# Kernel optimization log

Measured on AMD Instinct MI355X. Metric: run time of the kernel, lower is better.

Reference implementation:

```python
import jax, jax.numpy as jnp
import numpy as np

N = 20000          # num proposals (nodes)
E = 320000         # num edges
IN = 4096          # roi feature dim
EMB = 200          # glove embed dim
HID = 512          # hidden dim
NH = 8             # heads (conv1)
HC = HID // NH     # 64 per-head channels
NCLS = 151         # VG object classes
NEG_SLOPE = 0.2    # PyG GATConv leaky_relu slope


def setup_inputs() -> dict:
    key = jax.random.key(0)
    ks = jax.random.split(key, 18)
    d_in1 = IN + EMB + 128  # 4424, conv1 input dim
    inp = {
        "roi_features": jax.random.normal(ks[0], (N, IN), jnp.float32),
        "box_info": jax.random.uniform(ks[1], (N, 9), jnp.float32),
        # embedding tables
        "emb1": jax.random.normal(ks[2], (NCLS, EMB), jnp.float32) * 0.02,
        "emb2": jax.random.normal(ks[3], (NCLS, EMB), jnp.float32) * 0.02,
        # bbox MLP 9 -> 32 -> 128
        "bw1": jax.random.normal(ks[4], (9, 32), jnp.float32) / np.sqrt(9),
        "bb1": jnp.zeros((32,), jnp.float32),
        "bw2": jax.random.normal(ks[5], (32, 128), jnp.float32) / np.sqrt(32),
        "bb2": jnp.zeros((128,), jnp.float32),
        # GATConv1: d_in1 -> 8 heads x 64, concat
        "W1": jax.random.normal(ks[6], (d_in1, NH * HC), jnp.float32) / np.sqrt(d_in1),
        "a_src1": jax.random.normal(ks[7], (NH, HC), jnp.float32) * 0.1,
        "a_dst1": jax.random.normal(ks[8], (NH, HC), jnp.float32) * 0.1,
        "bias1": jnp.zeros((NH * HC,), jnp.float32),
        # GATConv2: 512 -> 512, 1 head, concat=False
        "W2": jax.random.normal(ks[9], (HID, HID), jnp.float32) / np.sqrt(HID),
        "a_src2": jax.random.normal(ks[10], (1, HID), jnp.float32) * 0.1,
        "a_dst2": jax.random.normal(ks[11], (1, HID), jnp.float32) * 0.1,
        "bias2": jnp.zeros((HID,), jnp.float32),
        # int inputs
        "obj_labels": jax.random.randint(ks[12], (N,), 0, NCLS, jnp.int32),
        "edge_index": jax.random.randint(ks[13], (2, E), 0, N, jnp.int32),
    }
    return inp


def _segment_softmax(logits, seg, n):
    # logits: [E, H]; softmax over edges sharing the same destination seg id
    m = jax.ops.segment_max(logits, seg, num_segments=n)
    e = jnp.exp(logits - m[seg])
    s = jax.ops.segment_sum(e, seg, num_segments=n)
    return e / (s[seg] + 1e-16)


def _gat_conv(x, src, dst, W, a_src, a_dst, bias, concat):
    # PyG GATConv (self-loops already included in src/dst); dropout off (eval)
    n = x.shape[0]
    H, C = a_src.shape
    h = (x @ W).reshape(n, H, C)                      # [N, H, C]
    al_s = jnp.einsum('nhc,hc->nh', h, a_src)         # [N, H]
    al_d = jnp.einsum('nhc,hc->nh', h, a_dst)
    logits = jax.nn.leaky_relu(al_s[src] + al_d[dst], NEG_SLOPE)  # [E, H]
    alpha = _segment_softmax(logits, dst, n)          # [E, H]
    out = jax.ops.segment_sum(alpha[:, :, None] * h[src], dst, num_segments=n)
    out = out.reshape(n, H * C) if concat else out.mean(axis=1)
    return out + bias


def reference(roi_features, box_info, emb1, emb2, bw1, bb1, bw2, bb2,
              W1, a_src1, a_dst1, bias1, W2, a_src2, a_dst2, bias2,
              obj_labels, edge_index):
    n = roi_features.shape[0]
    # predcls mode: GT labels -> embedding lookup
    obj_embed = emb1[obj_labels]                              # [N, 200]
    pos = jax.nn.relu(box_info @ bw1 + bb1)
    pos = jax.nn.relu(pos @ bw2 + bb2)                        # [N, 128]
    x = jnp.concatenate([roi_features, obj_embed, pos], -1)  # [N, 4424]

    # add self-loops (PyG GATConv default)
    ar = jnp.arange(n, dtype=edge_index.dtype)
    src = jnp.concatenate([edge_index[0], ar])
    dst = jnp.concatenate([edge_index[1], ar])

    edge_f1 = jax.nn.elu(_gat_conv(x, src, dst, W1, a_src1, a_dst1, bias1, True))
    obj_feats = _gat_conv(edge_f1, src, dst, W2, a_src2, a_dst2, bias2, False)

    obj_dists = jax.nn.one_hot(obj_labels, NCLS, dtype=jnp.float32)
    edge_pre_rep = jnp.concatenate([roi_features, obj_feats, emb2[obj_labels]], -1)
    return obj_dists, obj_labels, edge_pre_rep
```

## Files before the change

### kernel.cpp

```cpp
#include <hip/hip_runtime.h>
#include <hip/hip_bf16.h>

#define NNODES 20000
#define NEDGES 320000
#define ETOT   (NEDGES + NNODES)
#define KPADX  4224
#define SK     4
#define KC     (KPADX / SK)
#define MPAD   20096
#define NCLS   151
#define EPRW   4808
#define OUT_LAB_OFF  3020000L
#define OUT_EPR_OFF  3040000L
#define NSLOPE 0.2f
#define NGEMM1 2512
#define NCOPY  10000

typedef __attribute__((ext_vector_type(8))) short bf16x8;
typedef __attribute__((ext_vector_type(4))) float f32x4;
typedef __attribute__((ext_vector_type(4))) short s16x4;

__device__ __forceinline__ short f2bf(float v) {
  union { __hip_bfloat16 b; short s; } u;
  u.b = __float2bfloat16(v);
  return u.s;
}

__device__ __forceinline__ float bf2f(short s) {
  union { float f; unsigned u; } x;
  x.u = ((unsigned)(unsigned short)s) << 16;
  return x.f;
}

__device__ __forceinline__ void gld16(const short* g, short* l) {
  __builtin_amdgcn_global_load_lds(
      (const __attribute__((address_space(1))) unsigned int*)g,
      (__attribute__((address_space(3))) unsigned int*)l, 16, 0, 0);
}

#define QB0 5000
#define QB1 (QB0 + 5000)
#define QB2 (QB1 + 1584)
#define QB3 (QB2 + 2112)
#define QB4 (QB3 + 256)
#define QB5 (QB4 + 1329)
#define QB6 (QB5 + 151)

__global__ __launch_bounds__(256) void mega_prep_kernel(
    const float* __restrict__ roi, const float* __restrict__ box,
    const float* __restrict__ emb1, const float* __restrict__ emb2,
    const float* __restrict__ bw1, const float* __restrict__ bb1,
    const float* __restrict__ bw2, const float* __restrict__ bb2,
    const float* __restrict__ W1, const float* __restrict__ W2,
    const int* __restrict__ labels, const int* __restrict__ ei,
    short* __restrict__ x, short* __restrict__ w1t, short* __restrict__ w2t,
    short* __restrict__ ef1, int* __restrict__ deg,
    float* __restrict__ als2, float* __restrict__ ald2,
    float* __restrict__ E1, float* __restrict__ dout) {
  const int b = blockIdx.x;
  const int tid = threadIdx.x;

  __shared__ float hids[4][32];
  __shared__ float tile[32][33];

  if (b < QB0) {
    const int c0 = b * 2048 + tid;
    f32x4 v0[8], v1[8];
#pragma unroll
    for (int k = 0; k < 8; ++k) {
      const int c = c0 + k * 256;
      const float* src = &roi[((long)(c >> 9) << 12) + (c & 511) * 8];
      v0[k] = *(const f32x4*)src;
      v1[k] = *(const f32x4*)(src + 4);
    }
#pragma unroll
    for (int k = 0; k < 8; ++k) {
      const int c = c0 + k * 256;
      bf16x8 bb;
      bb[0] = f2bf(v0[k].x); bb[1] = f2bf(v0[k].y);
      bb[2] = f2bf(v0[k].z); bb[3] = f2bf(v0[k].w);
      bb[4] = f2bf(v1[k].x); bb[5] = f2bf(v1[k].y);
      bb[6] = f2bf(v1[k].z); bb[7] = f2bf(v1[k].w);
      __builtin_nontemporal_store(bb,
          (bf16x8*)&x[(long)(c >> 9) * KPADX + (c & 511) * 8]);
    }
  } else if (b < QB1) {
    const int w = tid >> 6;
    const int lane = tid & 63;
    const int nd = (b - QB0) * 4 + w;
    if (lane < 32) {
      float a = bb1[lane];
#pragma unroll
      for (int i = 0; i < 9; ++i) a += box[nd * 9 + i] * bw1[i * 32 + lane];
      hids[w][lane] = a > 0.f ? a : 0.f;
    }
    __syncthreads();
    const long xrow = (long)nd * KPADX;
#pragma unroll
    for (int jj = 0; jj < 2; ++jj) {
      const int j = lane + jj * 64;
      float a = bb2[j];
#pragma unroll
      for (int i = 0; i < 32; ++i) a += hids[w][i] * bw2[i * 128 + j];
      a = a > 0.f ? a : 0.f;
      x[xrow + 4096 + j] = f2bf(a);
    }
    const int lab = labels[nd];
    float* epr = dout + OUT_EPR_OFF + (long)nd * EPRW;
    if (lane < 50) {
      const f32x4 e2 = *(const f32x4*)&emb2[lab * 200 + lane * 4];
      __builtin_nontemporal_store(e2, (f32x4*)&epr[4608 + lane * 4]);
    }
    for (int j = lane; j < NCLS; j += 64)
      dout[(long)nd * NCLS + j] = (j == lab) ? 1.f : 0.f;
    if (lane == 0) dout[OUT_LAB_OFF + nd] = (float)lab;
  } else if (b < QB2) {
    const int t = (b - QB1) * 256 + tid;
    if (t < 96 * KPADX) x[(long)NNODES * KPADX + t] = 0;
    if (t < 96 * 512)   ef1[(long)NNODES * 512 + t] = 0;
    if (t < MPAD)       { als2[t] = 0.f; ald2[t] = 0.f; }
  } else if (b < QB3) {
    const int t = b - QB2;
    const int n0 = (t % 16) * 32;
    const int k0 = (t / 16) * 32;
    const int tx = tid & 31, ty = tid >> 5;
#pragma unroll
    for (int i = ty; i < 32; i += 8) {
      const int kp = k0 + i;
      const int src = kp < 4096 ? kp : kp + 200;
      tile[i][tx] = W1[(long)src * 512 + (n0 + tx)];
    }
    __syncthreads();
#pragma unroll
    for (int i = ty; i < 32; i += 8)
      w1t[(long)(n0 + i) * KPADX + (k0 + tx)] = f2bf(tile[tx][i]);
  } else if (b < QB4) {
    const int t = b - QB3;
    const int n0 = (t % 16) * 32;
    const int k0 = (t / 16) * 32;
    const int tx = tid & 31, ty = tid >> 5;
#pragma unroll
    for (int i = ty; i < 32; i += 8)
      tile[i][tx] = W2[(long)(k0 + i) * 512 + (n0 + tx)];
    __syncthreads();
#pragma unroll
    for (int i = ty; i < 32; i += 8)
      w2t[(long)(n0 + i) * 512 + (k0 + tx)] = f2bf(tile[tx][i]);
  } else if (b < QB5) {
    const int e = (b - QB4) * 256 + tid;
    if (e < ETOT) {
      const int d = (e < NEDGES) ? ei[NEDGES + e] : (e - NEDGES);
      atomicAdd(&deg[d], 1);
    }
  } else {
    const int c = b - QB5;
#pragma unroll
    for (int jj = 0; jj < 2; ++jj) {
      const int j = tid + jj * 256;
      float a = 0.f;
      for (int k = 0; k < 200; ++k)
        a += emb1[c * 200 + k] * W1[(long)(4096 + k) * 512 + j];
      E1[c * 512 + j] = a;
    }
  }
}

__global__ __launch_bounds__(256) void scan_kernel(const int* __restrict__ deg,
                                                   int* __restrict__ off,
                                                   int* __restrict__ cur) {
  __shared__ int part[256];
  const int tid = threadIdx.x;
  const int chunk = (NNODES + 255) / 256;
  int start = tid * chunk;
  int end = start + chunk; if (end > NNODES) end = NNODES;
  int s = 0;
  for (int i = start; i < end; ++i) s += deg[i];
  part[tid] = s;
  __syncthreads();
  for (int d = 1; d < 256; d <<= 1) {
    const int v = (tid >= d) ? part[tid - d] : 0;
    __syncthreads();
    part[tid] += v;
    __syncthreads();
  }
  int base = part[tid] - s;
  for (int i = start; i < end; ++i) { off[i] = base; cur[i] = base; base += deg[i]; }
}

__global__ void csr_fill_kernel(const int* __restrict__ ei, int* __restrict__ cur,
                                int* __restrict__ csrs) {
  const int e = blockIdx.x * 256 + threadIdx.x;
  if (e >= ETOT) return;
  const int s = (e < NEDGES) ? ei[e] : (e - NEDGES);
  const int d = (e < NEDGES) ? ei[NEDGES + e] : (e - NEDGES);
  unsigned slot = (unsigned)atomicAdd(&cur[d], 1);
  if (slot >= ETOT) slot = 0;
  csrs[slot] = s;
}

__global__ __launch_bounds__(256) void gemm_split(const short* __restrict__ A,
                                                  const short* __restrict__ BT,
                                                  short* __restrict__ hp,
                                                  const float* __restrict__ roi,
                                                  float* __restrict__ dout) {
  const int tid = threadIdx.x;
  if ((int)blockIdx.x >= NGEMM1) {
    const int t = (int)blockIdx.x - NGEMM1;
    const int c0 = t * 2048 + tid;
    f32x4 v[8];
#pragma unroll
    for (int k = 0; k < 8; ++k) {
      const int c = c0 + k * 256;
      v[k] = *(const f32x4*)&roi[((long)(c >> 10) << 12) + (c & 1023) * 4];
    }
#pragma unroll
    for (int k = 0; k < 8; ++k) {
      const int c = c0 + k * 256;
      __builtin_nontemporal_store(v[k],
          (f32x4*)&dout[OUT_EPR_OFF + (long)(c >> 10) * EPRW + (c & 1023) * 4]);
    }
    return;
  }
  __shared__ short As[4096];
  __shared__ short Bs[4096];
  const int lane = tid & 63;
  const int w = tid >> 6;
  const int wr = w >> 1, wc = w & 1;
  const int wid = (blockIdx.x & 7) * 314 + ((int)blockIdx.x >> 3);
  const long bm = (long)(wid >> 4) * 128;
  const int  sk = (wid >> 2) & 3;
  const long bn = (long)(wid & 3) * 128;

  f32x4 acc[4][4] = {};

  const short* gA0 = A + (bm + w * 32 + (lane >> 2)) * (long)KPADX + sk * KC + (lane & 3) * 8;
  const short* gA1 = gA0 + 16L * KPADX;
  const short* gB0 = BT + (bn + w * 32 + (lane >> 2)) * (long)KPADX + sk * KC + (lane & 3) * 8;
  const short* gB1 = gB0 + 16L * KPADX;
  short* lA0 = &As[w * 1024];
  short* lA1 = &As[w * 1024 + 512];
  short* lB0 = &Bs[w * 1024];
  short* lB1 = &Bs[w * 1024 + 512];

  const int ar = (wr * 64 + (lane & 15)) * 32 + (lane >> 4) * 8;
  const int br = (wc * 64 + (lane & 15)) * 32 + (lane >> 4) * 8;

  for (int k0 = 0; k0 < KC; k0 += 32) {
    gld16(gA0, lA0); gld16(gA1, lA1);
    gld16(gB0, lB0); gld16(gB1, lB1);
    gA0 += 32; gA1 += 32; gB0 += 32; gB1 += 32;
    asm volatile("s_waitcnt vmcnt(0)" ::: "memory");
    __syncthreads();
    bf16x8 a[4], b[4];
#pragma unroll
    for (int mi = 0; mi < 4; ++mi) a[mi] = *(const bf16x8*)&As[ar + mi * 512];
#pragma unroll
    for (int ni = 0; ni < 4; ++ni) b[ni] = *(const bf16x8*)&Bs[br + ni * 512];
#pragma unroll
    for (int mi = 0; mi < 4; ++mi)
#pragma unroll
      for (int ni = 0; ni < 4; ++ni)
        acc[mi][ni] = __builtin_amdgcn_mfma_f32_16x16x32_bf16(a[mi], b[ni], acc[mi][ni], 0, 0, 0);
    __syncthreads();
  }

  short* Cp = hp + (long)sk * MPAD * 512;
#pragma unroll
  for (int mi = 0; mi < 4; ++mi) {
#pragma unroll
    for (int ni = 0; ni < 4; ++ni) {
      const long row0 = bm + wr * 64 + mi * 16 + (lane >> 4) * 4;
      const long col  = bn + wc * 64 + ni * 16 + (lane & 15);
#pragma unroll
      for (int r = 0; r < 4; ++r)
        Cp[(row0 + r) * 512 + col] = f2bf(acc[mi][ni][r]);
    }
  }
}

__global__ __launch_bounds__(256) void reduce1_kernel(short* __restrict__ hp,
    const float* __restrict__ E1, const int* __restrict__ labels,
    const float* __restrict__ aS, const float* __restrict__ aD,
    float* __restrict__ als, float* __restrict__ ald) {
  const int row = blockIdx.x * 4 + (threadIdx.x >> 6);
  const int lane = threadIdx.x & 63;
  const int c0 = lane * 8;
  const long base = (long)row * 512 + c0;
  float v[8] = {};
#pragma unroll
  for (int s = 0; s < SK; ++s) {
    const bf16x8 p = *(const bf16x8*)&hp[(long)s * MPAD * 512 + base];
#pragma unroll
    for (int j = 0; j < 8; ++j) v[j] += bf2f(p[j]);
  }
  const int lab = (row < NNODES) ? labels[row] : 0;
  const float* e1r = E1 + (long)lab * 512;
#pragma unroll
  for (int j = 0; j < 8; ++j) v[j] += e1r[c0 + j];
  bf16x8 o;
#pragma unroll
  for (int j = 0; j < 8; ++j) o[j] = f2bf(v[j]);
  *(bf16x8*)&hp[base] = o;
  float s_ = 0.f, d_ = 0.f;
#pragma unroll
  for (int j = 0; j < 8; ++j) {
    s_ += v[j] * aS[c0 + j];
    d_ += v[j] * aD[c0 + j];
  }
#pragma unroll
  for (int oo = 1; oo < 8; oo <<= 1) {
    s_ += __shfl_xor(s_, oo);
    d_ += __shfl_xor(d_, oo);
  }
  if ((lane & 7) == 0) {
    const int head = lane >> 3;
    als[row * 8 + head] = s_;
    ald[row * 8 + head] = d_;
  }
}

__global__ __launch_bounds__(256) void gemm_bt(const short* __restrict__ A,
                                               const short* __restrict__ BT,
                                               short* __restrict__ C,
                                               const float* __restrict__ aS,
                                               const float* __restrict__ aD,
                                               float* __restrict__ als,
                                               float* __restrict__ ald,
                                               int Kpad, int Ncols, int H) {
  __shared__ short As[4096];
  __shared__ short Bs[4096];
  const int tid = threadIdx.x;
  const int lane = tid & 63;
  const int w = tid >> 6;
  const int wr = w >> 1, wc = w & 1;
  const int nbn = Ncols >> 7;
  const long bm = (long)((int)blockIdx.x / nbn) * 128;
  const long bn = (long)((int)blockIdx.x % nbn) * 128;

  f32x4 acc[4][4] = {};

  const short* gA0 = A + (bm + w * 32 + (lane >> 2)) * (long)Kpad + (lane & 3) * 8;
  const short* gA1 = gA0 + 16L * Kpad;
  const short* gB0 = BT + (bn + w * 32 + (lane >> 2)) * (long)Kpad + (lane & 3) * 8;
  const short* gB1 = gB0 + 16L * Kpad;
  short* lA0 = &As[w * 1024];
  short* lA1 = &As[w * 1024 + 512];
  short* lB0 = &Bs[w * 1024];
  short* lB1 = &Bs[w * 1024 + 512];

  const int ar = (wr * 64 + (lane & 15)) * 32 + (lane >> 4) * 8;
  const int br = (wc * 64 + (lane & 15)) * 32 + (lane >> 4) * 8;

  for (int k0 = 0; k0 < Kpad; k0 += 32) {
    gld16(gA0, lA0); gld16(gA1, lA1);
    gld16(gB0, lB0); gld16(gB1, lB1);
    gA0 += 32; gA1 += 32; gB0 += 32; gB1 += 32;
    asm volatile("s_waitcnt vmcnt(0)" ::: "memory");
    __syncthreads();
    bf16x8 a[4], b[4];
#pragma unroll
    for (int mi = 0; mi < 4; ++mi) a[mi] = *(const bf16x8*)&As[ar + mi * 512];
#pragma unroll
    for (int ni = 0; ni < 4; ++ni) b[ni] = *(const bf16x8*)&Bs[br + ni * 512];
#pragma unroll
    for (int mi = 0; mi < 4; ++mi)
#pragma unroll
      for (int ni = 0; ni < 4; ++ni)
        acc[mi][ni] = __builtin_amdgcn_mfma_f32_16x16x32_bf16(a[mi], b[ni], acc[mi][ni], 0, 0, 0);
    __syncthreads();
  }

  const int colb = (int)bn + wc * 64 + (lane & 15);

#pragma unroll
  for (int mi = 0; mi < 4; ++mi) {
#pragma unroll
    for (int ni = 0; ni < 4; ++ni) {
      const long row0 = bm + wr * 64 + mi * 16 + (lane >> 4) * 4;
      const long col  = bn + wc * 64 + ni * 16 + (lane & 15);
#pragma unroll
      for (int r = 0; r < 4; ++r)
        C[(row0 + r) * (long)Ncols + col] = f2bf(acc[mi][ni][r]);
    }
  }

  float asv[4], adv[4];
#pragma unroll
  for (int ni = 0; ni < 4; ++ni) {
    asv[ni] = aS[colb + ni * 16];
    adv[ni] = aD[colb + ni * 16];
  }
  const int head = (H == 8) ? (((int)bn >> 6) + wc) : 0;
#pragma unroll
  for (int mi = 0; mi < 4; ++mi) {
#pragma unroll
    for (int r = 0; r < 4; ++r) {
      float s = 0.f, d = 0.f;
#pragma unroll
      for (int ni = 0; ni < 4; ++ni) {
        const float v = acc[mi][ni][r];
        s += v * asv[ni];
        d += v * adv[ni];
      }
#pragma unroll
      for (int o = 1; o < 16; o <<= 1) {
        s += __shfl_xor(s, o);
        d += __shfl_xor(d, o);
      }
      if ((lane & 15) == 0) {
        const long row = bm + wr * 64 + mi * 16 + (lane >> 4) * 4 + r;
        atomicAdd(&als[row * H + head], s);
        atomicAdd(&ald[row * H + head], d);
      }
    }
  }
}

__global__ __launch_bounds__(256) void gather1_kernel(const int* __restrict__ off,
    const int* __restrict__ csrs,
    const float* __restrict__ als, const float* __restrict__ ald,
    const short* __restrict__ h1, const float* __restrict__ bias,
    short* __restrict__ ef1) {
  const int dn = blockIdx.x * 4 + (threadIdx.x >> 6);
  const int lane = threadIdx.x & 63;
  const int c0 = lane * 8;
  const int head = lane >> 3;
  const int beg = off[dn];
  const int end = (dn == NNODES - 1) ? ETOT : off[dn + 1];
  const float ad = ald[dn * 8 + head];
  float sum = 0.f;
  float acc[8] = {};
  for (int i = beg; i < end; ++i) {
    int s = csrs[i];
    if ((unsigned)s >= NNODES) s = 0;
    float l = als[s * 8 + head] + ad;
    l = l > 0.f ? l : NSLOPE * l;
    const float wgt = expf(l);
    sum += wgt;
    const bf16x8 hv = *(const bf16x8*)&h1[(long)s * 512 + c0];
#pragma unroll
    for (int j = 0; j < 8; ++j) acc[j] += wgt * bf2f(hv[j]);
  }
  const float inv = 1.f / (sum + 1e-16f);
  bf16x8 outv;
#pragma unroll
  for (int j = 0; j < 8; ++j) {
    float r = acc[j] * inv + bias[c0 + j];
    r = r > 0.f ? r : expm1f(r);
    outv[j] = f2bf(r);
  }
  *(bf16x8*)&ef1[(long)dn * 512 + c0] = outv;
}

__global__ __launch_bounds__(256) void gather2_kernel(const int* __restrict__ off,
    const int* __restrict__ csrs,
    const float* __restrict__ als, const float* __restrict__ ald,
    const short* __restrict__ h2, const float* __restrict__ bias,
    float* __restrict__ dout) {
  const int dn = blockIdx.x * 4 + (threadIdx.x >> 6);
  const int lane = threadIdx.x & 63;
  const int c0 = lane * 8;
  const int beg = off[dn];
  const int end = (dn == NNODES - 1) ? ETOT : off[dn + 1];
  const float ad = ald[dn];
  float sum = 0.f;
  float acc[8] = {};
  for (int i = beg; i < end; ++i) {
    int s = csrs[i];
    if ((unsigned)s >= NNODES) s = 0;
    float l = als[s] + ad;
    l = l > 0.f ? l : NSLOPE * l;
    const float wgt = expf(l);
    sum += wgt;
    const bf16x8 hv = *(const bf16x8*)&h2[(long)s * 512 + c0];
#pragma unroll
    for (int j = 0; j < 8; ++j) acc[j] += wgt * bf2f(hv[j]);
  }
  const float inv = 1.f / (sum + 1e-16f);
  float* epr = dout + OUT_EPR_OFF + (long)dn * EPRW + 4096;
  f32x4 o0, o1;
  o0.x = acc[0] * inv + bias[c0 + 0];
  o0.y = acc[1] * inv + bias[c0 + 1];
  o0.z = acc[2] * inv + bias[c0 + 2];
  o0.w = acc[3] * inv + bias[c0 + 3];
  o1.x = acc[4] * inv + bias[c0 + 4];
  o1.y = acc[5] * inv + bias[c0 + 5];
  o1.z = acc[6] * inv + bias[c0 + 6];
  o1.w = acc[7] * inv + bias[c0 + 7];
  __builtin_nontemporal_store(o0, (f32x4*)&epr[c0]);
  __builtin_nontemporal_store(o1, (f32x4*)&epr[c0 + 4]);
}

extern "C" void kernel_launch(void* const* d_in, const int* in_sizes, int n_in,
                              void* d_out, int out_size, void* d_ws, size_t ws_size,
                              hipStream_t stream) {
  const float* roi  = (const float*)d_in[0];
  const float* box  = (const float*)d_in[1];
  const float* emb1 = (const float*)d_in[2];
  const float* emb2 = (const float*)d_in[3];
  const float* bw1  = (const float*)d_in[4];
  const float* bb1  = (const float*)d_in[5];
  const float* bw2  = (const float*)d_in[6];
  const float* bb2  = (const float*)d_in[7];
  const float* W1   = (const float*)d_in[8];
  const float* as1  = (const float*)d_in[9];
  const float* ad1  = (const float*)d_in[10];
  const float* b1   = (const float*)d_in[11];
  const float* W2   = (const float*)d_in[12];
  const float* as2  = (const float*)d_in[13];
  const float* ad2  = (const float*)d_in[14];
  const float* b2   = (const float*)d_in[15];
  const int* labels = (const int*)d_in[16];
  const int* ei     = (const int*)d_in[17];
  float* dout = (float*)d_out;

  char* wsb = (char*)d_ws;
  size_t o = 0;
  auto alloc = [&](size_t bytes) -> void* {
    void* p = wsb + o;
    o += (bytes + 255) & ~(size_t)255;
    return p;
  };
  short* x    = (short*)alloc((size_t)MPAD * KPADX * 2);
  short* w1t  = (short*)alloc((size_t)512 * KPADX * 2);
  short* hp   = (short*)alloc((size_t)SK * MPAD * 512 * 2);
  short* h1   = hp;
  short* ef1  = (short*)alloc((size_t)MPAD * 512 * 2);
  short* w2t  = (short*)alloc((size_t)512 * 512 * 2);
  short* h2   = (short*)alloc((size_t)MPAD * 512 * 2);
  float* als1 = (float*)alloc((size_t)MPAD * 8 * 4);
  float* ald1 = (float*)alloc((size_t)MPAD * 8 * 4);
  float* als2 = (float*)alloc((size_t)MPAD * 4);
  float* ald2 = (float*)alloc((size_t)MPAD * 4);
  float* E1   = (float*)alloc((size_t)NCLS * 512 * 4);
  int*   deg  = (int*)alloc((size_t)NNODES * 4);
  int*   offs = (int*)alloc((size_t)NNODES * 4);
  int*   cur  = (int*)alloc((size_t)NNODES * 4);
  int*   csrs = (int*)alloc((size_t)ETOT * 4);

  const int EB = (ETOT + 255) / 256;

  hipMemsetAsync(deg, 0, (size_t)NNODES * 4, stream);

  hipLaunchKernelGGL(mega_prep_kernel, dim3(QB6), dim3(256), 0, stream,
                     roi, box, emb1, emb2, bw1, bb1, bw2, bb2, W1, W2,
                     labels, ei, x, w1t, w2t, ef1, deg,
                     als2, ald2, E1, dout);
  hipLaunchKernelGGL(scan_kernel, dim3(1), dim3(256), 0, stream, deg, offs, cur);
  hipLaunchKernelGGL(csr_fill_kernel, dim3(EB), dim3(256), 0, stream, ei, cur, csrs);
  hipLaunchKernelGGL(gemm_split, dim3(NGEMM1 + NCOPY), dim3(256), 0, stream,
                     x, w1t, hp, roi, dout);
  hipLaunchKernelGGL(reduce1_kernel, dim3(MPAD / 4), dim3(256), 0, stream,
                     hp, E1, labels, as1, ad1, als1, ald1);
  hipLaunchKernelGGL(gather1_kernel, dim3(NNODES / 4), dim3(256), 0, stream,
                     offs, csrs, als1, ald1, h1, b1, ef1);
  hipLaunchKernelGGL(gemm_bt, dim3(157 * 4), dim3(256), 0, stream,
                     ef1, w2t, h2, as2, ad2, als2, ald2, 512, 512, 1);
  hipLaunchKernelGGL(gather2_kernel, dim3(NNODES / 4), dim3(256), 0, stream,
                     offs, csrs, als2, ald2, h2, b2, dout);
}
```

Measured before the change: 606.3 us.

## Double-buffer LDS in both GEMMs and move roi copy into prep kernel

```diff
diff --git a/kernel.cpp b/kernel.cpp
--- a/kernel.cpp
+++ b/kernel.cpp
@@ -13,8 +13,6 @@
 #define OUT_LAB_OFF  3020000L
 #define OUT_EPR_OFF  3040000L
 #define NSLOPE 0.2f
-#define NGEMM1 2512
-#define NCOPY  10000
 
 typedef __attribute__((ext_vector_type(8))) short bf16x8;
 typedef __attribute__((ext_vector_type(4))) float f32x4;
@@ -38,13 +36,14 @@
       (__attribute__((address_space(3))) unsigned int*)l, 16, 0, 0);
 }
 
-#define QB0 5000
-#define QB1 (QB0 + 5000)
-#define QB2 (QB1 + 1584)
-#define QB3 (QB2 + 2112)
-#define QB4 (QB3 + 256)
-#define QB5 (QB4 + 1329)
-#define QB6 (QB5 + 151)
+#define QB0  5000
+#define QB0b (QB0 + 10000)
+#define QB1  (QB0b + 5000)
+#define QB2  (QB1 + 1584)
+#define QB3  (QB2 + 2112)
+#define QB4  (QB3 + 256)
+#define QB5  (QB4 + 1329)
+#define QB6  (QB5 + 151)
 
 __global__ __launch_bounds__(256) void mega_prep_kernel(
     const float* __restrict__ roi, const float* __restrict__ box,
@@ -84,10 +83,25 @@
       __builtin_nontemporal_store(bb,
           (bf16x8*)&x[(long)(c >> 9) * KPADX + (c & 511) * 8]);
     }
+  } else if (b < QB0b) {
+    const int t = b - QB0;
+    const int c0 = t * 2048 + tid;
+    f32x4 v[8];
+#pragma unroll
+    for (int k = 0; k < 8; ++k) {
+      const int c = c0 + k * 256;
+      v[k] = *(const f32x4*)&roi[((long)(c >> 10) << 12) + (c & 1023) * 4];
+    }
+#pragma unroll
+    for (int k = 0; k < 8; ++k) {
+      const int c = c0 + k * 256;
+      __builtin_nontemporal_store(v[k],
+          (f32x4*)&dout[OUT_EPR_OFF + (long)(c >> 10) * EPRW + (c & 1023) * 4]);
+    }
   } else if (b < QB1) {
     const int w = tid >> 6;
     const int lane = tid & 63;
-    const int nd = (b - QB0) * 4 + w;
+    const int nd = (b - QB0b) * 4 + w;
     if (lane < 32) {
       float a = bb1[lane];
 #pragma unroll
@@ -200,29 +214,10 @@
 
 __global__ __launch_bounds__(256) void gemm_split(const short* __restrict__ A,
                                                   const short* __restrict__ BT,
-                                                  short* __restrict__ hp,
-                                                  const float* __restrict__ roi,
-                                                  float* __restrict__ dout) {
+                                                  short* __restrict__ hp) {
+  __shared__ short As[2][4096];
+  __shared__ short Bs[2][4096];
   const int tid = threadIdx.x;
-  if ((int)blockIdx.x >= NGEMM1) {
-    const int t = (int)blockIdx.x - NGEMM1;
-    const int c0 = t * 2048 + tid;
-    f32x4 v[8];
-#pragma unroll
-    for (int k = 0; k < 8; ++k) {
-      const int c = c0 + k * 256;
-      v[k] = *(const f32x4*)&roi[((long)(c >> 10) << 12) + (c & 1023) * 4];
-    }
-#pragma unroll
-    for (int k = 0; k < 8; ++k) {
-      const int c = c0 + k * 256;
-      __builtin_nontemporal_store(v[k],
-          (f32x4*)&dout[OUT_EPR_OFF + (long)(c >> 10) * EPRW + (c & 1023) * 4]);
-    }
-    return;
-  }
-  __shared__ short As[4096];
-  __shared__ short Bs[4096];
   const int lane = tid & 63;
   const int w = tid >> 6;
   const int wr = w >> 1, wc = w & 1;
@@ -237,31 +232,39 @@
   const short* gA1 = gA0 + 16L * KPADX;
   const short* gB0 = BT + (bn + w * 32 + (lane >> 2)) * (long)KPADX + sk * KC + (lane & 3) * 8;
   const short* gB1 = gB0 + 16L * KPADX;
-  short* lA0 = &As[w * 1024];
-  short* lA1 = &As[w * 1024 + 512];
-  short* lB0 = &Bs[w * 1024];
-  short* lB1 = &Bs[w * 1024 + 512];
-
+
+  const int lofs = w * 1024;
   const int ar = (wr * 64 + (lane & 15)) * 32 + (lane >> 4) * 8;
   const int br = (wc * 64 + (lane & 15)) * 32 + (lane >> 4) * 8;
 
-  for (int k0 = 0; k0 < KC; k0 += 32) {
-    gld16(gA0, lA0); gld16(gA1, lA1);
-    gld16(gB0, lB0); gld16(gB1, lB1);
-    gA0 += 32; gA1 += 32; gB0 += 32; gB1 += 32;
-    asm volatile("s_waitcnt vmcnt(0)" ::: "memory");
-    __syncthreads();
+  gld16(gA0, &As[0][lofs]); gld16(gA1, &As[0][lofs + 512]);
+  gld16(gB0, &Bs[0][lofs]); gld16(gB1, &Bs[0][lofs + 512]);
+  gA0 += 32; gA1 += 32; gB0 += 32; gB1 += 32;
+
+  const int NT = KC / 32;
+  int cur = 0;
+  for (int t = 0; t < NT; ++t) {
+    if (t + 1 < NT) {
+      gld16(gA0, &As[cur ^ 1][lofs]); gld16(gA1, &As[cur ^ 1][lofs + 512]);
+      gld16(gB0, &Bs[cur ^ 1][lofs]); gld16(gB1, &Bs[cur ^ 1][lofs + 512]);
+      gA0 += 32; gA1 += 32; gB0 += 32; gB1 += 32;
+      asm volatile("s_waitcnt vmcnt(4)" ::: "memory");
+    } else {
+      asm volatile("s_waitcnt vmcnt(0)" ::: "memory");
+    }
+    __builtin_amdgcn_s_barrier();
     bf16x8 a[4], b[4];
 #pragma unroll
-    for (int mi = 0; mi < 4; ++mi) a[mi] = *(const bf16x8*)&As[ar + mi * 512];
-#pragma unroll
-    for (int ni = 0; ni < 4; ++ni) b[ni] = *(const bf16x8*)&Bs[br + ni * 512];
+    for (int mi = 0; mi < 4; ++mi) a[mi] = *(const bf16x8*)&As[cur][ar + mi * 512];
+#pragma unroll
+    for (int ni = 0; ni < 4; ++ni) b[ni] = *(const bf16x8*)&Bs[cur][br + ni * 512];
 #pragma unroll
     for (int mi = 0; mi < 4; ++mi)
 #pragma unroll
       for (int ni = 0; ni < 4; ++ni)
         acc[mi][ni] = __builtin_amdgcn_mfma_f32_16x16x32_bf16(a[mi], b[ni], acc[mi][ni], 0, 0, 0);
-    __syncthreads();
+    __builtin_amdgcn_s_barrier();
+    cur ^= 1;
   }
 
   short* Cp = hp + (long)sk * MPAD * 512;
@@ -327,8 +330,8 @@
                                                float* __restrict__ als,
                                                float* __restrict__ ald,
                                                int Kpad, int Ncols, int H) {
-  __shared__ short As[4096];
-  __shared__ short Bs[4096];
+  __shared__ short As[2][4096];
+  __shared__ short Bs[2][4096];
   const int tid = threadIdx.x;
   const int lane = tid & 63;
   const int w = tid >> 6;
@@ -343,31 +346,39 @@
   const short* gA1 = gA0 + 16L * Kpad;
   const short* gB0 = BT + (bn + w * 32 + (lane >> 2)) * (long)Kpad + (lane & 3) * 8;
   const short* gB1 = gB0 + 16L * Kpad;
-  short* lA0 = &As[w * 1024];
-  short* lA1 = &As[w * 1024 + 512];
-  short* lB0 = &Bs[w * 1024];
-  short* lB1 = &Bs[w * 1024 + 512];
-
+
+  const int lofs = w * 1024;
   const int ar = (wr * 64 + (lane & 15)) * 32 + (lane >> 4) * 8;
   const int br = (wc * 64 + (lane & 15)) * 32 + (lane >> 4) * 8;
 
-  for (int k0 = 0; k0 < Kpad; k0 += 32) {
-    gld16(gA0, lA0); gld16(gA1, lA1);
-    gld16(gB0, lB0); gld16(gB1, lB1);
-    gA0 += 32; gA1 += 32; gB0 += 32; gB1 += 32;
-    asm volatile("s_waitcnt vmcnt(0)" ::: "memory");
-    __syncthreads();
+  gld16(gA0, &As[0][lofs]); gld16(gA1, &As[0][lofs + 512]);
+  gld16(gB0, &Bs[0][lofs]); gld16(gB1, &Bs[0][lofs + 512]);
+  gA0 += 32; gA1 += 32; gB0 += 32; gB1 += 32;
+
+  const int NT = Kpad / 32;
+  int cur = 0;
+  for (int t = 0; t < NT; ++t) {
+    if (t + 1 < NT) {
+      gld16(gA0, &As[cur ^ 1][lofs]); gld16(gA1, &As[cur ^ 1][lofs + 512]);
+      gld16(gB0, &Bs[cur ^ 1][lofs]); gld16(gB1, &Bs[cur ^ 1][lofs + 512]);
+      gA0 += 32; gA1 += 32; gB0 += 32; gB1 += 32;
+      asm volatile("s_waitcnt vmcnt(4)" ::: "memory");
+    } else {
+      asm volatile("s_waitcnt vmcnt(0)" ::: "memory");
+    }
+    __builtin_amdgcn_s_barrier();
     bf16x8 a[4], b[4];
 #pragma unroll
-    for (int mi = 0; mi < 4; ++mi) a[mi] = *(const bf16x8*)&As[ar + mi * 512];
-#pragma unroll
-    for (int ni = 0; ni < 4; ++ni) b[ni] = *(const bf16x8*)&Bs[br + ni * 512];
+    for (int mi = 0; mi < 4; ++mi) a[mi] = *(const bf16x8*)&As[cur][ar + mi * 512];
+#pragma unroll
+    for (int ni = 0; ni < 4; ++ni) b[ni] = *(const bf16x8*)&Bs[cur][br + ni * 512];
 #pragma unroll
     for (int mi = 0; mi < 4; ++mi)
 #pragma unroll
       for (int ni = 0; ni < 4; ++ni)
         acc[mi][ni] = __builtin_amdgcn_mfma_f32_16x16x32_bf16(a[mi], b[ni], acc[mi][ni], 0, 0, 0);
-    __syncthreads();
+    __builtin_amdgcn_s_barrier();
+    cur ^= 1;
   }
 
   const int colb = (int)bn + wc * 64 + (lane & 15);
@@ -548,8 +559,8 @@
                      als2, ald2, E1, dout);
   hipLaunchKernelGGL(scan_kernel, dim3(1), dim3(256), 0, stream, deg, offs, cur);
   hipLaunchKernelGGL(csr_fill_kernel, dim3(EB), dim3(256), 0, stream, ei, cur, csrs);
-  hipLaunchKernelGGL(gemm_split, dim3(NGEMM1 + NCOPY), dim3(256), 0, stream,
-                     x, w1t, hp, roi, dout);
+  hipLaunchKernelGGL(gemm_split, dim3(157 * SK * 4), dim3(256), 0, stream,
+                     x, w1t, hp);
   hipLaunchKernelGGL(reduce1_kernel, dim3(MPAD / 4), dim3(256), 0, stream,
                      hp, E1, labels, as1, ad1, als1, ald1);
   hipLaunchKernelGGL(gather1_kernel, dim3(NNODES / 4), dim3(256), 0, stream,
```

Result: slower. 621.2 us (+2.5%).
